# Performance work log

Measured on AMD Instinct MI355X. Metric: run time of the kernel, lower is better.

The kernel has to match this reference:

```python
import jax, jax.numpy as jnp
import numpy as np

B, N, C = 16, 65536, 21          # batch, anchors, classes (class 0 = background)
TH_CONF = 0.05                   # confidence threshold
TH_IOU = 0.5                     # NMS IoU threshold
TOP_K = 200                      # candidates kept per (batch, class) before NMS
V0, V1 = 0.1, 0.2                # SSD box-coder variances


def setup_inputs() -> dict:
    key = jax.random.key(0)
    k1, k2, k3, k4 = jax.random.split(key, 4)
    conf = jax.random.normal(k1, (B, N, C), dtype=jnp.float32)
    loc = jax.random.normal(k2, (B, N, 4), dtype=jnp.float32)
    # anchors in center form (cx, cy, w, h), normalized coords
    cxcy = jax.random.uniform(k3, (N, 2), dtype=jnp.float32)
    wh = 0.02 + 0.2 * jax.random.uniform(k4, (N, 2), dtype=jnp.float32)
    anchors = jnp.concatenate([cxcy, wh], axis=-1)
    return {"conf": conf, "loc": loc, "anchors": anchors}


def _decode(anchors, loc):
    # SSD decode: anchors [N,4] center form, loc [B,N,4] offsets -> [B,N,4] xyxy
    a_xy, a_wh = anchors[:, :2], anchors[:, 2:]
    xy = a_xy + loc[..., :2] * V0 * a_wh
    wh = a_wh * jnp.exp(loc[..., 2:] * V1)
    return jnp.concatenate([xy - 0.5 * wh, xy + 0.5 * wh], axis=-1)


def _iou(boxes):
    # boxes [K,4] xyxy -> pairwise IoU [K,K]
    area = jnp.maximum(boxes[:, 2] - boxes[:, 0], 0.0) * jnp.maximum(boxes[:, 3] - boxes[:, 1], 0.0)
    lt = jnp.maximum(boxes[:, None, :2], boxes[None, :, :2])
    rb = jnp.minimum(boxes[:, None, 2:], boxes[None, :, 2:])
    wh = jnp.maximum(rb - lt, 0.0)
    inter = wh[..., 0] * wh[..., 1]
    union = area[:, None] + area[None, :] - inter
    return inter / jnp.maximum(union, 1e-9)


def _nms_keep(iou, valid):
    # greedy NMS over score-sorted candidates; valid = (score >= TH_CONF)
    K = iou.shape[0]
    idx = jnp.arange(K)

    def body(keep, xs):
        row, v, i = xs
        suppressed = jnp.any((row > TH_IOU) & keep & (idx < i))
        k = v & (~suppressed)
        return keep.at[i].set(k), 0

    keep, _ = jax.lax.scan(body, jnp.zeros((K,), dtype=bool), (iou, valid, idx))
    return keep


def reference(conf, loc, anchors):
    score = jax.nn.softmax(conf, axis=2)            # [B,N,C]
    boxes = _decode(anchors, loc)                   # [B,N,4]
    # skip background class 0 (cls_base = 1 for softmax classifier)
    cls_scores = jnp.swapaxes(score[..., 1:], 1, 2)  # [B,C-1,N]
    top_s, top_i = jax.lax.top_k(cls_scores, TOP_K)  # [B,C-1,K], sorted desc
    top_boxes = jax.vmap(lambda bx, ix: bx[ix])(boxes, top_i)  # [B,C-1,K,4]
    valid = top_s >= TH_CONF
    keep = jax.vmap(jax.vmap(lambda b, v: _nms_keep(_iou(b), v)))(top_boxes, valid)  # [B,C-1,K]
    out_boxes = jnp.where(keep[..., None], top_boxes, 0.0)
    out_scores = jnp.where(keep, top_s, 0.0)
    return jnp.concatenate([out_boxes, out_scores[..., None]], axis=-1)  # [B,C-1,K,5]
```

## Files before the change

kernel.cpp:

```cpp
#include <hip/hip_runtime.h>
#include <stdint.h>

#define NB     16
#define NANCH  65536
#define NC     21
#define NCLS   20
#define NCOL   (NB * NCLS)
#define TOPK   200
#define NBINS  1024
#define CAP    256
#define CAPCOL 4096
#define CAPLDS 2048
#define CNTSTRIDE 16
#define NPAIRS 19900

constexpr float TH      = 0.05f;
constexpr float TPRE    = 0.20f;
constexpr float SCALE20 = (float)NBINS / 0.80f;
constexpr float SCALE05 = (float)NBINS / 0.95f;

__device__ __forceinline__ int bin20(float s) {
  int b = (int)((s - 0.20f) * SCALE20);
  return b < 0 ? 0 : (b > NBINS - 1 ? NBINS - 1 : b);
}
__device__ __forceinline__ int bin05(float s) {
  int b = (int)((s - 0.05f) * SCALE05);
  return b < 0 ? 0 : (b > NBINS - 1 ? NBINS - 1 : b);
}

__device__ __forceinline__ unsigned long long shflx64(unsigned long long v, int m) {
  unsigned int lo = (unsigned int)v, hi = (unsigned int)(v >> 32);
  lo = __shfl_xor(lo, m);
  hi = __shfl_xor(hi, m);
  return ((unsigned long long)hi << 32) | lo;
}
__device__ __forceinline__ unsigned long long rl64(unsigned long long v, int lane) {
  unsigned int lo = __builtin_amdgcn_readlane((int)(unsigned int)v, lane);
  unsigned int hi = __builtin_amdgcn_readlane((int)(unsigned int)(v >> 32), lane);
  return ((unsigned long long)hi << 32) | lo;
}

__device__ __forceinline__ void softmax_tail(const float* x, float* e, float& S) {
  float m = x[0];
#pragma unroll
  for (int c = 1; c < NC; ++c) m = fmaxf(m, x[c]);
#pragma unroll
  for (int c = 0; c < NC; ++c) e[c] = expf(x[c] - m);
  float r0 = e[0] + e[8],  r1 = e[1] + e[9],  r2 = e[2] + e[10], r3 = e[3] + e[11];
  float r4 = e[4] + e[12], r5 = e[5] + e[13], r6 = e[6] + e[14], r7 = e[7] + e[15];
  S = ((r0 + r1) + (r2 + r3)) + ((r4 + r5) + (r6 + r7));
  S += e[16]; S += e[17]; S += e[18]; S += e[19]; S += e[20];
}

__global__ __launch_bounds__(256) void softmax_collect_kernel(
    const float* __restrict__ conf,
    unsigned int* __restrict__ cnt, unsigned long long* __restrict__ cand) {
  const int tid = threadIdx.x;
  __shared__ float ld[256 * NC];
  const float4* src = (const float4*)conf + (long long)blockIdx.x * 1344;
  float4* dst4 = (float4*)ld;
#pragma unroll
  for (int i = 0; i < 5; ++i) dst4[tid + i * 256] = src[tid + i * 256];
  if (tid < 64) dst4[tid + 1280] = src[tid + 1280];
  __syncthreads();

  const int a = blockIdx.x * 256 + tid;
  const int b = a >> 16;
  const int n = a & (NANCH - 1);
  float x[NC];
#pragma unroll
  for (int c = 0; c < NC; ++c) x[c] = ld[tid * NC + c];
  float e[NC], S;
  softmax_tail(x, e, S);
  const float t = TPRE * S;
  unsigned int takemask = 0;
#pragma unroll
  for (int c = 0; c < NCLS; ++c)
    if (e[c + 1] >= t) takemask |= (1u << c);

  __shared__ unsigned int wcnt[4][NCLS];
  __shared__ unsigned int wbase[4][NCLS];
  const int wave = tid >> 6, lane = tid & 63;
#pragma unroll
  for (int c = 0; c < NCLS; ++c) {
    unsigned long long m = __ballot((takemask >> c) & 1);
    if (lane == 0) wcnt[wave][c] = (unsigned int)__popcll(m);
  }
  __syncthreads();
  if (tid < NCLS) {
    const int c = tid;
    unsigned int t0 = wcnt[0][c], t1 = wcnt[1][c], t2 = wcnt[2][c], t3 = wcnt[3][c];
    unsigned int tot = t0 + t1 + t2 + t3;
    unsigned int base = tot ? atomicAdd(&cnt[(b * NCLS + c) * CNTSTRIDE], tot) : 0u;
    wbase[0][c] = base;
    wbase[1][c] = base + t0;
    wbase[2][c] = base + t0 + t1;
    wbase[3][c] = base + t0 + t1 + t2;
  }
  __syncthreads();
#pragma unroll
  for (int c = 0; c < NCLS; ++c) {
    bool take = (takemask >> c) & 1;
    unsigned long long m = __ballot(take);
    if (take) {
      float s = e[c + 1] / S;
      unsigned int off = wbase[wave][c] +
                         (unsigned int)__popcll(m & ((1ULL << lane) - 1));
      if (off < CAPCOL) {
        unsigned int key = __float_as_uint(s) | 0x80000000u;
        cand[(long long)(b * NCLS + c) * CAPCOL + off] =
            ((unsigned long long)(key ^ 0xFFFFFFFFu) << 32) |
            (unsigned long long)(unsigned int)n;
      }
    }
  }
}

__device__ __forceinline__ int find_sel(unsigned int* hist, unsigned int* part,
                                        int* s_sel, int tid) {
  unsigned int p = hist[tid*4] + hist[tid*4+1] + hist[tid*4+2] + hist[tid*4+3];
  part[tid] = p;
  if (tid == 0) *s_sel = -1;
  __syncthreads();
  if (tid < 64) {
    unsigned int p4 = part[tid*4] + part[tid*4+1] + part[tid*4+2] + part[tid*4+3];
    unsigned int sfx = p4;
#pragma unroll
    for (int off = 1; off < 64; off <<= 1) {
      unsigned int o = __shfl_down(sfx, off);
      if (tid + off < 64) sfx += o;
    }
    unsigned int above = sfx - p4;
    if (above < TOPK && sfx >= TOPK) {
      unsigned int cum = above; int sel = tid * 16; bool found = false;
      for (int q = 3; q >= 0 && !found; --q) {
        unsigned int pc = part[tid*4 + q];
        if (cum + pc >= TOPK) {
          for (int i = 3; i >= 0; --i) {
            unsigned int c = hist[(tid*4+q)*4 + i];
            if (cum + c >= TOPK) { sel = (tid*4+q)*4 + i; found = true; break; }
            cum += c;
          }
        } else cum += pc;
      }
      *s_sel = sel;
    }
  }
  __syncthreads();
  return *s_sel;
}

__global__ __launch_bounds__(256) void topk_nms_kernel(
    const unsigned long long* __restrict__ candg,
    const unsigned int* __restrict__ cnt,
    const float* __restrict__ conf, const float* __restrict__ loc,
    const float* __restrict__ anchors, float* __restrict__ out) {
  const int bc = blockIdx.x;
  const int b  = bc / NCLS;
  const int cls = bc % NCLS;
  const int tid = threadIdx.x;

  __shared__ unsigned long long cg_lds[CAPLDS];
  __shared__ unsigned int hist[NBINS];
  __shared__ unsigned int part[256];
  __shared__ int s_sel, s_n;
  __shared__ unsigned long long cand[CAP];
  __shared__ float bx[TOPK][5];
  __shared__ float barea[TOPK];
  __shared__ unsigned long long adj[TOPK][4];
  __shared__ unsigned long long keptw[4];

  int nc = (int)cnt[bc * CNTSTRIDE];
  const bool fast = (nc >= TOPK && nc <= CAPLDS);
  for (int i = tid; i < NBINS; i += 256) hist[i] = 0;
  if (tid == 0) s_n = 0;
  for (int i = tid; i < TOPK * 4; i += 256) ((unsigned long long*)adj)[i] = 0;

  const unsigned long long* cg = candg + (long long)bc * CAPCOL;
  if (fast) {
    const int npair = nc >> 1;
    const ulonglong2* cg2 = (const ulonglong2*)cg;
    for (int i = tid; i < npair; i += 256) {
      ulonglong2 v2 = cg2[i];
      cg_lds[2 * i]     = v2.x;
      cg_lds[2 * i + 1] = v2.y;
    }
    if ((nc & 1) && tid == 0) cg_lds[nc - 1] = cg[nc - 1];
    __syncthreads();
    for (int i = tid; i < nc; i += 256) {
      unsigned int key = (unsigned int)(cg_lds[i] >> 32) ^ 0xFFFFFFFFu;
      float s = __uint_as_float(key ^ 0x80000000u);
      atomicAdd(&hist[bin20(s)], 1u);
    }
    __syncthreads();
    int sel = find_sel(hist, part, &s_sel, tid);
    for (int i = tid; i < nc; i += 256) {
      unsigned long long k64 = cg_lds[i];
      unsigned int key = (unsigned int)(k64 >> 32) ^ 0xFFFFFFFFu;
      float s = __uint_as_float(key ^ 0x80000000u);
      if (bin20(s) >= sel) {
        int pos = atomicAdd(&s_n, 1);
        if (pos < CAP) cand[pos] = k64;
      }
    }
  } else {
    __syncthreads();
    for (int n = tid; n < NANCH; n += 256) {
      const float* row = conf + ((long long)b * NANCH + n) * NC;
      float x[NC], e[NC], S;
#pragma unroll
      for (int c = 0; c < NC; ++c) x[c] = row[c];
      softmax_tail(x, e, S);
      float s = e[cls + 1] / S;
      if (s >= TH) atomicAdd(&hist[bin05(s)], 1u);
    }
    __syncthreads();
    int sel = find_sel(hist, part, &s_sel, tid);
    for (int n = tid; n < NANCH; n += 256) {
      const float* row = conf + ((long long)b * NANCH + n) * NC;
      float x[NC], e[NC], S;
#pragma unroll
      for (int c = 0; c < NC; ++c) x[c] = row[c];
      softmax_tail(x, e, S);
      float s = e[cls + 1] / S;
      if (s >= TH && (sel < 0 || bin05(s) >= sel)) {
        int pos = atomicAdd(&s_n, 1);
        if (pos < CAP) {
          unsigned int key = __float_as_uint(s) | 0x80000000u;
          cand[pos] = ((unsigned long long)(key ^ 0xFFFFFFFFu) << 32) |
                      (unsigned long long)(unsigned int)n;
        }
      }
    }
  }
  __syncthreads();
  int ncand = s_n; if (ncand > CAP) ncand = CAP;

  unsigned long long v = (tid < ncand) ? cand[tid] : ~0ULL;
  for (int k = 2; k <= CAP; k <<= 1) {
    const bool up = ((tid & k) == 0);
    for (int j = k >> 1; j >= 64; j >>= 1) {
      cand[tid] = v;
      __syncthreads();
      unsigned long long o = cand[tid ^ j];
      bool keepMin = (((tid & j) == 0) == up);
      v = ((v < o) == keepMin) ? v : o;
      __syncthreads();
    }
    for (int j = (k >> 1) < 32 ? (k >> 1) : 32; j >= 1; j >>= 1) {
      unsigned long long o = shflx64(v, j);
      bool keepMin = (((tid & j) == 0) == up);
      v = ((v < o) == keepMin) ? v : o;
    }
  }
  const int nsel = (ncand < TOPK) ? ncand : TOPK;

  if (tid < TOPK) {
    if (tid < nsel) {
      unsigned int key = (unsigned int)(v >> 32) ^ 0xFFFFFFFFu;
      float s = __uint_as_float(key ^ 0x80000000u);
      int idx = (int)(unsigned int)(v & 0xFFFFFFFFu);
      float4 anc = ((const float4*)anchors)[idx];
      float4 l   = ((const float4*)loc)[(long long)b * NANCH + idx];
      float cx = anc.x + (l.x * 0.1f) * anc.z;
      float cy = anc.y + (l.y * 0.1f) * anc.w;
      float w  = anc.z * expf(l.z * 0.2f);
      float h  = anc.w * expf(l.w * 0.2f);
      float x1 = cx - 0.5f * w, y1 = cy - 0.5f * h;
      float x2 = cx + 0.5f * w, y2 = cy + 0.5f * h;
      bx[tid][0] = x1; bx[tid][1] = y1; bx[tid][2] = x2; bx[tid][3] = y2;
      bx[tid][4] = s;
      barea[tid] = fmaxf(x2 - x1, 0.0f) * fmaxf(y2 - y1, 0.0f);
    } else {
      bx[tid][0] = bx[tid][1] = bx[tid][2] = bx[tid][3] = bx[tid][4] = 0.0f;
      barea[tid] = 0.0f;
    }
  }
  __syncthreads();

  for (int p = tid; p < NPAIRS; p += 256) {
    float xr = (399.0f - sqrtf((float)(159201 - 8 * p))) * 0.5f;
    int i = (int)xr;
    if (i > 198) i = 198;
    while (i * (399 - i) / 2 > p) --i;
    while ((i + 1) * (398 - i) / 2 <= p) ++i;
    int j = i + 1 + (p - i * (399 - i) / 2);
    float ltx = fmaxf(bx[i][0], bx[j][0]);
    float lty = fmaxf(bx[i][1], bx[j][1]);
    float rbx = fminf(bx[i][2], bx[j][2]);
    float rby = fminf(bx[i][3], bx[j][3]);
    float iw = fmaxf(rbx - ltx, 0.0f);
    float ih = fmaxf(rby - lty, 0.0f);
    float inter = iw * ih;
    float uni = barea[i] + barea[j] - inter;
    float um = fmaxf(uni, 1e-9f);
    float half = 0.5f * um;
    bool hit;
    if (inter > half * 1.000001f)      hit = true;
    else if (inter < half * 0.999999f) hit = false;
    else                               hit = (inter / um > 0.5f);
    if (hit) atomicOr(&adj[i][j >> 6], 1ULL << (j & 63));
  }
  __syncthreads();

  if (tid < 64) {
    const int l = tid;
    unsigned long long r0[4], r1[4], r2[4], r3[4];
#pragma unroll
    for (int w = 0; w < 4; ++w) {
      r0[w] = adj[l][w];
      r1[w] = adj[l + 64][w];
      r2[w] = (l < 72) ? adj[l + 128][w] : 0ULL;
      r3[w] = (l < 8)  ? adj[l + 192][w] : 0ULL;
    }
    unsigned long long sup0 = 0, sup1 = 0, sup2 = 0, sup3 = 0;
    unsigned long long k0 = 0, k1 = 0, k2 = 0, k3 = 0;
    for (int ii = 0; ii < 64; ++ii) {
      bool kept = (ii < nsel) && !((sup0 >> ii) & 1ULL);
      if (kept) {
        k0 |= 1ULL << ii;
        sup0 |= rl64(r0[0], ii); sup1 |= rl64(r0[1], ii);
        sup2 |= rl64(r0[2], ii); sup3 |= rl64(r0[3], ii);
      }
    }
    for (int ii = 0; ii < 64; ++ii) {
      bool kept = ((64 + ii) < nsel) && !((sup1 >> ii) & 1ULL);
      if (kept) {
        k1 |= 1ULL << ii;
        sup1 |= rl64(r1[1], ii); sup2 |= rl64(r1[2], ii);
        sup3 |= rl64(r1[3], ii);
      }
    }
    for (int ii = 0; ii < 64; ++ii) {
      bool kept = ((128 + ii) < nsel) && !((sup2 >> ii) & 1ULL);
      if (kept) {
        k2 |= 1ULL << ii;
        sup2 |= rl64(r2[2], ii); sup3 |= rl64(r2[3], ii);
      }
    }
    for (int ii = 0; ii < 8; ++ii) {
      bool kept = ((192 + ii) < nsel) && !((sup3 >> ii) & 1ULL);
      if (kept) { k3 |= 1ULL << ii; sup3 |= rl64(r3[3], ii); }
    }
    if (l == 0) { keptw[0] = k0; keptw[1] = k1; keptw[2] = k2; keptw[3] = k3; }
  }
  __syncthreads();

  if (tid < TOPK) {
    float* o = out + ((long long)bc * TOPK + tid) * 5;
    bool k = (keptw[tid >> 6] >> (tid & 63)) & 1ULL;
    o[0] = k ? bx[tid][0] : 0.0f;
    o[1] = k ? bx[tid][1] : 0.0f;
    o[2] = k ? bx[tid][2] : 0.0f;
    o[3] = k ? bx[tid][3] : 0.0f;
    o[4] = k ? bx[tid][4] : 0.0f;
  }
}

extern "C" void kernel_launch(void* const* d_in, const int* in_sizes, int n_in,
                              void* d_out, int out_size, void* d_ws, size_t ws_size,
                              hipStream_t stream) {
  const float* conf    = (const float*)d_in[0];
  const float* loc     = (const float*)d_in[1];
  const float* anchors = (const float*)d_in[2];
  float* out = (float*)d_out;

  char* ws = (char*)d_ws;
  unsigned long long* cand = (unsigned long long*)ws;
  unsigned int*       cnt  = (unsigned int*)(ws + 10485760);

  hipMemsetAsync(ws + 10485760, 0, 320 * CNTSTRIDE * 4, stream);
  softmax_collect_kernel<<<(NB * NANCH) / 256, 256, 0, stream>>>(conf, cnt, cand);
  topk_nms_kernel<<<NCOL, 256, 0, stream>>>(cand, cnt, conf, loc, anchors, out);
}
```

Measured before the change: 99.64 us.

## Pack two (batch,class) columns per 512-thread block and alias NMS buffers onto staging LDS

The top-k/NMS kernel now runs two columns per block, with 512 threads split into halves, so 160 blocks are launched instead of 320. The adjacency matrix, box and area arrays are moved into the candidate staging buffer, which is no longer needed at that point, to keep total LDS use down. The fast path is taken only when both columns qualify, so one slow column drags its partner through the full softmax rescan. Block-wide barriers are now shared by both halves, coupling their progress.

Result: slower. 104.0 us (+4.4%).

```diff
diff --git a/kernel.cpp b/kernel.cpp
--- a/kernel.cpp
+++ b/kernel.cpp
@@ -117,28 +117,28 @@
 }
 
 __device__ __forceinline__ int find_sel(unsigned int* hist, unsigned int* part,
-                                        int* s_sel, int tid) {
-  unsigned int p = hist[tid*4] + hist[tid*4+1] + hist[tid*4+2] + hist[tid*4+3];
-  part[tid] = p;
-  if (tid == 0) *s_sel = -1;
-  __syncthreads();
-  if (tid < 64) {
-    unsigned int p4 = part[tid*4] + part[tid*4+1] + part[tid*4+2] + part[tid*4+3];
+                                        int* s_sel, int t) {
+  unsigned int p = hist[t*4] + hist[t*4+1] + hist[t*4+2] + hist[t*4+3];
+  part[t] = p;
+  if (t == 0) *s_sel = -1;
+  __syncthreads();
+  if (t < 64) {
+    unsigned int p4 = part[t*4] + part[t*4+1] + part[t*4+2] + part[t*4+3];
     unsigned int sfx = p4;
 #pragma unroll
     for (int off = 1; off < 64; off <<= 1) {
       unsigned int o = __shfl_down(sfx, off);
-      if (tid + off < 64) sfx += o;
+      if (t + off < 64) sfx += o;
     }
     unsigned int above = sfx - p4;
     if (above < TOPK && sfx >= TOPK) {
-      unsigned int cum = above; int sel = tid * 16; bool found = false;
+      unsigned int cum = above; int sel = t * 16; bool found = false;
       for (int q = 3; q >= 0 && !found; --q) {
-        unsigned int pc = part[tid*4 + q];
+        unsigned int pc = part[t*4 + q];
         if (cum + pc >= TOPK) {
           for (int i = 3; i >= 0; --i) {
-            unsigned int c = hist[(tid*4+q)*4 + i];
-            if (cum + c >= TOPK) { sel = (tid*4+q)*4 + i; found = true; break; }
+            unsigned int c = hist[(t*4+q)*4 + i];
+            if (cum + c >= TOPK) { sel = (t*4+q)*4 + i; found = true; break; }
             cum += c;
           }
         } else cum += pc;
@@ -150,73 +150,76 @@
   return *s_sel;
 }
 
-__global__ __launch_bounds__(256) void topk_nms_kernel(
+__global__ __launch_bounds__(512) void topk_nms_kernel(
     const unsigned long long* __restrict__ candg,
     const unsigned int* __restrict__ cnt,
     const float* __restrict__ conf, const float* __restrict__ loc,
     const float* __restrict__ anchors, float* __restrict__ out) {
-  const int bc = blockIdx.x;
-  const int b  = bc / NCLS;
-  const int cls = bc % NCLS;
-  const int tid = threadIdx.x;
-
-  __shared__ unsigned long long cg_lds[CAPLDS];
-  __shared__ unsigned int hist[NBINS];
-  __shared__ unsigned int part[256];
-  __shared__ int s_sel, s_n;
-  __shared__ unsigned long long cand[CAP];
-  __shared__ float bx[TOPK][5];
-  __shared__ float barea[TOPK];
-  __shared__ unsigned long long adj[TOPK][4];
-  __shared__ unsigned long long keptw[4];
+  const int tid  = threadIdx.x;
+  const int half = tid >> 8;
+  const int t    = tid & 255;
+  const int bc   = blockIdx.x * 2 + half;
+  const int b    = bc / NCLS;
+  const int cls  = bc % NCLS;
+
+  __shared__ unsigned long long cg_lds[2][CAPLDS];
+  __shared__ unsigned int hist[2][NBINS];
+  __shared__ unsigned int part[2][256];
+  __shared__ int s_sel[2], s_n[2];
+  __shared__ unsigned long long cand[2][CAP];
+  __shared__ unsigned long long keptw[2][4];
+  unsigned long long* adj  = &cg_lds[half][0];
+  float*              bx   = (float*)&cg_lds[half][800];
+  float*              brea = (float*)&cg_lds[half][800] + 1000;
 
   int nc = (int)cnt[bc * CNTSTRIDE];
-  const bool fast = (nc >= TOPK && nc <= CAPLDS);
-  for (int i = tid; i < NBINS; i += 256) hist[i] = 0;
-  if (tid == 0) s_n = 0;
-  for (int i = tid; i < TOPK * 4; i += 256) ((unsigned long long*)adj)[i] = 0;
+  int nc_other = (int)cnt[(blockIdx.x * 2 + (half ^ 1)) * CNTSTRIDE];
+  const bool fastpair = (nc >= TOPK && nc <= CAPLDS) &&
+                        (nc_other >= TOPK && nc_other <= CAPLDS);
+  for (int i = t; i < NBINS; i += 256) hist[half][i] = 0;
+  if (t == 0) s_n[half] = 0;
 
   const unsigned long long* cg = candg + (long long)bc * CAPCOL;
-  if (fast) {
+  if (fastpair) {
     const int npair = nc >> 1;
     const ulonglong2* cg2 = (const ulonglong2*)cg;
-    for (int i = tid; i < npair; i += 256) {
+    for (int i = t; i < npair; i += 256) {
       ulonglong2 v2 = cg2[i];
-      cg_lds[2 * i]     = v2.x;
-      cg_lds[2 * i + 1] = v2.y;
-    }
-    if ((nc & 1) && tid == 0) cg_lds[nc - 1] = cg[nc - 1];
+      cg_lds[half][2 * i]     = v2.x;
+      cg_lds[half][2 * i + 1] = v2.y;
+    }
+    if ((nc & 1) && t == 0) cg_lds[half][nc - 1] = cg[nc - 1];
     __syncthreads();
-    for (int i = tid; i < nc; i += 256) {
-      unsigned int key = (unsigned int)(cg_lds[i] >> 32) ^ 0xFFFFFFFFu;
+    for (int i = t; i < nc; i += 256) {
+      unsigned int key = (unsigned int)(cg_lds[half][i] >> 32) ^ 0xFFFFFFFFu;
       float s = __uint_as_float(key ^ 0x80000000u);
-      atomicAdd(&hist[bin20(s)], 1u);
+      atomicAdd(&hist[half][bin20(s)], 1u);
     }
     __syncthreads();
-    int sel = find_sel(hist, part, &s_sel, tid);
-    for (int i = tid; i < nc; i += 256) {
-      unsigned long long k64 = cg_lds[i];
+    int sel = find_sel(hist[half], part[half], &s_sel[half], t);
+    for (int i = t; i < nc; i += 256) {
+      unsigned long long k64 = cg_lds[half][i];
       unsigned int key = (unsigned int)(k64 >> 32) ^ 0xFFFFFFFFu;
       float s = __uint_as_float(key ^ 0x80000000u);
       if (bin20(s) >= sel) {
-        int pos = atomicAdd(&s_n, 1);
-        if (pos < CAP) cand[pos] = k64;
+        int pos = atomicAdd(&s_n[half], 1);
+        if (pos < CAP) cand[half][pos] = k64;
       }
     }
   } else {
     __syncthreads();
-    for (int n = tid; n < NANCH; n += 256) {
+    for (int n = t; n < NANCH; n += 256) {
       const float* row = conf + ((long long)b * NANCH + n) * NC;
       float x[NC], e[NC], S;
 #pragma unroll
       for (int c = 0; c < NC; ++c) x[c] = row[c];
       softmax_tail(x, e, S);
       float s = e[cls + 1] / S;
-      if (s >= TH) atomicAdd(&hist[bin05(s)], 1u);
+      if (s >= TH) atomicAdd(&hist[half][bin05(s)], 1u);
     }
     __syncthreads();
-    int sel = find_sel(hist, part, &s_sel, tid);
-    for (int n = tid; n < NANCH; n += 256) {
+    int sel = find_sel(hist[half], part[half], &s_sel[half], t);
+    for (int n = t; n < NANCH; n += 256) {
       const float* row = conf + ((long long)b * NANCH + n) * NC;
       float x[NC], e[NC], S;
 #pragma unroll
@@ -224,39 +227,40 @@
       softmax_tail(x, e, S);
       float s = e[cls + 1] / S;
       if (s >= TH && (sel < 0 || bin05(s) >= sel)) {
-        int pos = atomicAdd(&s_n, 1);
+        int pos = atomicAdd(&s_n[half], 1);
         if (pos < CAP) {
           unsigned int key = __float_as_uint(s) | 0x80000000u;
-          cand[pos] = ((unsigned long long)(key ^ 0xFFFFFFFFu) << 32) |
-                      (unsigned long long)(unsigned int)n;
+          cand[half][pos] = ((unsigned long long)(key ^ 0xFFFFFFFFu) << 32) |
+                            (unsigned long long)(unsigned int)n;
         }
       }
     }
   }
   __syncthreads();
-  int ncand = s_n; if (ncand > CAP) ncand = CAP;
-
-  unsigned long long v = (tid < ncand) ? cand[tid] : ~0ULL;
+  int ncand = s_n[half]; if (ncand > CAP) ncand = CAP;
+
+  unsigned long long v = (t < ncand) ? cand[half][t] : ~0ULL;
   for (int k = 2; k <= CAP; k <<= 1) {
-    const bool up = ((tid & k) == 0);
+    const bool up = ((t & k) == 0);
     for (int j = k >> 1; j >= 64; j >>= 1) {
-      cand[tid] = v;
+      cand[half][t] = v;
       __syncthreads();
-      unsigned long long o = cand[tid ^ j];
-      bool keepMin = (((tid & j) == 0) == up);
+      unsigned long long o = cand[half][t ^ j];
+      bool keepMin = (((t & j) == 0) == up);
       v = ((v < o) == keepMin) ? v : o;
       __syncthreads();
     }
     for (int j = (k >> 1) < 32 ? (k >> 1) : 32; j >= 1; j >>= 1) {
       unsigned long long o = shflx64(v, j);
-      bool keepMin = (((tid & j) == 0) == up);
+      bool keepMin = (((t & j) == 0) == up);
       v = ((v < o) == keepMin) ? v : o;
     }
   }
   const int nsel = (ncand < TOPK) ? ncand : TOPK;
 
-  if (tid < TOPK) {
-    if (tid < nsel) {
+  for (int i = t; i < TOPK * 4; i += 256) adj[i] = 0;
+  if (t < TOPK) {
+    if (t < nsel) {
       unsigned int key = (unsigned int)(v >> 32) ^ 0xFFFFFFFFu;
       float s = __uint_as_float(key ^ 0x80000000u);
       int idx = (int)(unsigned int)(v & 0xFFFFFFFFu);
@@ -268,50 +272,50 @@
       float h  = anc.w * expf(l.w * 0.2f);
       float x1 = cx - 0.5f * w, y1 = cy - 0.5f * h;
       float x2 = cx + 0.5f * w, y2 = cy + 0.5f * h;
-      bx[tid][0] = x1; bx[tid][1] = y1; bx[tid][2] = x2; bx[tid][3] = y2;
-      bx[tid][4] = s;
-      barea[tid] = fmaxf(x2 - x1, 0.0f) * fmaxf(y2 - y1, 0.0f);
+      bx[t * 5 + 0] = x1; bx[t * 5 + 1] = y1;
+      bx[t * 5 + 2] = x2; bx[t * 5 + 3] = y2; bx[t * 5 + 4] = s;
+      brea[t] = fmaxf(x2 - x1, 0.0f) * fmaxf(y2 - y1, 0.0f);
     } else {
-      bx[tid][0] = bx[tid][1] = bx[tid][2] = bx[tid][3] = bx[tid][4] = 0.0f;
-      barea[tid] = 0.0f;
-    }
-  }
-  __syncthreads();
-
-  for (int p = tid; p < NPAIRS; p += 256) {
+      bx[t*5+0] = bx[t*5+1] = bx[t*5+2] = bx[t*5+3] = bx[t*5+4] = 0.0f;
+      brea[t] = 0.0f;
+    }
+  }
+  __syncthreads();
+
+  for (int p = t; p < NPAIRS; p += 256) {
     float xr = (399.0f - sqrtf((float)(159201 - 8 * p))) * 0.5f;
     int i = (int)xr;
     if (i > 198) i = 198;
     while (i * (399 - i) / 2 > p) --i;
     while ((i + 1) * (398 - i) / 2 <= p) ++i;
     int j = i + 1 + (p - i * (399 - i) / 2);
-    float ltx = fmaxf(bx[i][0], bx[j][0]);
-    float lty = fmaxf(bx[i][1], bx[j][1]);
-    float rbx = fminf(bx[i][2], bx[j][2]);
-    float rby = fminf(bx[i][3], bx[j][3]);
+    float ltx = fmaxf(bx[i*5+0], bx[j*5+0]);
+    float lty = fmaxf(bx[i*5+1], bx[j*5+1]);
+    float rbx = fminf(bx[i*5+2], bx[j*5+2]);
+    float rby = fminf(bx[i*5+3], bx[j*5+3]);
     float iw = fmaxf(rbx - ltx, 0.0f);
     float ih = fmaxf(rby - lty, 0.0f);
     float inter = iw * ih;
-    float uni = barea[i] + barea[j] - inter;
+    float uni = brea[i] + brea[j] - inter;
     float um = fmaxf(uni, 1e-9f);
-    float half = 0.5f * um;
+    float half_u = 0.5f * um;
     bool hit;
-    if (inter > half * 1.000001f)      hit = true;
-    else if (inter < half * 0.999999f) hit = false;
-    else                               hit = (inter / um > 0.5f);
-    if (hit) atomicOr(&adj[i][j >> 6], 1ULL << (j & 63));
-  }
-  __syncthreads();
-
-  if (tid < 64) {
-    const int l = tid;
+    if (inter > half_u * 1.000001f)      hit = true;
+    else if (inter < half_u * 0.999999f) hit = false;
+    else                                 hit = (inter / um > 0.5f);
+    if (hit) atomicOr(&adj[i * 4 + (j >> 6)], 1ULL << (j & 63));
+  }
+  __syncthreads();
+
+  if (t < 64) {
+    const int l = t;
     unsigned long long r0[4], r1[4], r2[4], r3[4];
 #pragma unroll
     for (int w = 0; w < 4; ++w) {
-      r0[w] = adj[l][w];
-      r1[w] = adj[l + 64][w];
-      r2[w] = (l < 72) ? adj[l + 128][w] : 0ULL;
-      r3[w] = (l < 8)  ? adj[l + 192][w] : 0ULL;
+      r0[w] = adj[l * 4 + w];
+      r1[w] = adj[(l + 64) * 4 + w];
+      r2[w] = (l < 72) ? adj[(l + 128) * 4 + w] : 0ULL;
+      r3[w] = (l < 8)  ? adj[(l + 192) * 4 + w] : 0ULL;
     }
     unsigned long long sup0 = 0, sup1 = 0, sup2 = 0, sup3 = 0;
     unsigned long long k0 = 0, k1 = 0, k2 = 0, k3 = 0;
@@ -342,18 +346,19 @@
       bool kept = ((192 + ii) < nsel) && !((sup3 >> ii) & 1ULL);
       if (kept) { k3 |= 1ULL << ii; sup3 |= rl64(r3[3], ii); }
     }
-    if (l == 0) { keptw[0] = k0; keptw[1] = k1; keptw[2] = k2; keptw[3] = k3; }
-  }
-  __syncthreads();
-
-  if (tid < TOPK) {
-    float* o = out + ((long long)bc * TOPK + tid) * 5;
-    bool k = (keptw[tid >> 6] >> (tid & 63)) & 1ULL;
-    o[0] = k ? bx[tid][0] : 0.0f;
-    o[1] = k ? bx[tid][1] : 0.0f;
-    o[2] = k ? bx[tid][2] : 0.0f;
-    o[3] = k ? bx[tid][3] : 0.0f;
-    o[4] = k ? bx[tid][4] : 0.0f;
+    if (l == 0) { keptw[half][0] = k0; keptw[half][1] = k1;
+                  keptw[half][2] = k2; keptw[half][3] = k3; }
+  }
+  __syncthreads();
+
+  if (t < TOPK) {
+    float* o = out + ((long long)bc * TOPK + t) * 5;
+    bool k = (keptw[half][t >> 6] >> (t & 63)) & 1ULL;
+    o[0] = k ? bx[t*5+0] : 0.0f;
+    o[1] = k ? bx[t*5+1] : 0.0f;
+    o[2] = k ? bx[t*5+2] : 0.0f;
+    o[3] = k ? bx[t*5+3] : 0.0f;
+    o[4] = k ? bx[t*5+4] : 0.0f;
   }
 }
 
@@ -371,5 +376,5 @@
 
   hipMemsetAsync(ws + 10485760, 0, 320 * CNTSTRIDE * 4, stream);
   softmax_collect_kernel<<<(NB * NANCH) / 256, 256, 0, stream>>>(conf, cnt, cand);
-  topk_nms_kernel<<<NCOL, 256, 0, stream>>>(cand, cnt, conf, loc, anchors, out);
-}
+  topk_nms_kernel<<<NCOL / 2, 512, 0, stream>>>(cand, cnt, conf, loc, anchors, out);
+}
```

## Compute IoU adjacency rows per thread without atomics and branchless NMS scan

Applied to the files above, without the earlier changes.

Replaces the triangular pair-index decomposition (sqrt plus fix-up loops and atomicOr into shared memory) with one thread per row that builds each 64-bit adjacency word in registers and stores it directly. This removes the zero-init of adj, the LDS atomics and the pair-index arithmetic. In exchange only 200 of 256 threads do the IoU work and each does 200 serial iterations. The greedy NMS scan is made branchless with masks, and the output write is coalesced as a flat loop over TOPK*5 floats.

After: 98.65 us. No clear change (-1.0%).

```diff
diff --git a/kernel.cpp b/kernel.cpp
--- a/kernel.cpp
+++ b/kernel.cpp
@@ -12,7 +12,6 @@
 #define CAPCOL 4096
 #define CAPLDS 2048
 #define CNTSTRIDE 16
-#define NPAIRS 19900
 
 constexpr float TH      = 0.05f;
 constexpr float TPRE    = 0.20f;
@@ -165,7 +164,7 @@
   __shared__ unsigned int part[256];
   __shared__ int s_sel, s_n;
   __shared__ unsigned long long cand[CAP];
-  __shared__ float bx[TOPK][5];
+  __shared__ float bxf[TOPK * 5];
   __shared__ float barea[TOPK];
   __shared__ unsigned long long adj[TOPK][4];
   __shared__ unsigned long long keptw[4];
@@ -174,7 +173,6 @@
   const bool fast = (nc >= TOPK && nc <= CAPLDS);
   for (int i = tid; i < NBINS; i += 256) hist[i] = 0;
   if (tid == 0) s_n = 0;
-  for (int i = tid; i < TOPK * 4; i += 256) ((unsigned long long*)adj)[i] = 0;
 
   const unsigned long long* cg = candg + (long long)bc * CAPCOL;
   if (fast) {
@@ -268,38 +266,48 @@
       float h  = anc.w * expf(l.w * 0.2f);
       float x1 = cx - 0.5f * w, y1 = cy - 0.5f * h;
       float x2 = cx + 0.5f * w, y2 = cy + 0.5f * h;
-      bx[tid][0] = x1; bx[tid][1] = y1; bx[tid][2] = x2; bx[tid][3] = y2;
-      bx[tid][4] = s;
+      bxf[tid * 5 + 0] = x1; bxf[tid * 5 + 1] = y1;
+      bxf[tid * 5 + 2] = x2; bxf[tid * 5 + 3] = y2; bxf[tid * 5 + 4] = s;
       barea[tid] = fmaxf(x2 - x1, 0.0f) * fmaxf(y2 - y1, 0.0f);
     } else {
-      bx[tid][0] = bx[tid][1] = bx[tid][2] = bx[tid][3] = bx[tid][4] = 0.0f;
+      bxf[tid*5+0] = bxf[tid*5+1] = bxf[tid*5+2] = bxf[tid*5+3] = bxf[tid*5+4] = 0.0f;
       barea[tid] = 0.0f;
     }
   }
   __syncthreads();
 
-  for (int p = tid; p < NPAIRS; p += 256) {
-    float xr = (399.0f - sqrtf((float)(159201 - 8 * p))) * 0.5f;
-    int i = (int)xr;
-    if (i > 198) i = 198;
-    while (i * (399 - i) / 2 > p) --i;
-    while ((i + 1) * (398 - i) / 2 <= p) ++i;
-    int j = i + 1 + (p - i * (399 - i) / 2);
-    float ltx = fmaxf(bx[i][0], bx[j][0]);
-    float lty = fmaxf(bx[i][1], bx[j][1]);
-    float rbx = fminf(bx[i][2], bx[j][2]);
-    float rby = fminf(bx[i][3], bx[j][3]);
-    float iw = fmaxf(rbx - ltx, 0.0f);
-    float ih = fmaxf(rby - lty, 0.0f);
-    float inter = iw * ih;
-    float uni = barea[i] + barea[j] - inter;
-    float um = fmaxf(uni, 1e-9f);
-    float half = 0.5f * um;
-    bool hit;
-    if (inter > half * 1.000001f)      hit = true;
-    else if (inter < half * 0.999999f) hit = false;
-    else                               hit = (inter / um > 0.5f);
-    if (hit) atomicOr(&adj[i][j >> 6], 1ULL << (j & 63));
+  if (tid < TOPK) {
+    const float ax1 = bxf[tid*5+0], ay1 = bxf[tid*5+1];
+    const float ax2 = bxf[tid*5+2], ay2 = bxf[tid*5+3];
+    const float aar = barea[tid];
+#pragma unroll
+    for (int w = 0; w < 4; ++w) {
+      const int jend = (w < 3) ? 64 : (TOPK - 192);
+      unsigned long long roww = 0;
+      for (int jj = 0; jj < jend; ++jj) {
+        const int j = w * 64 + jj;
+        float jx1 = bxf[j*5+0], jy1 = bxf[j*5+1];
+        float jx2 = bxf[j*5+2], jy2 = bxf[j*5+3];
+        float jar = barea[j];
+        float ltx = fmaxf(ax1, jx1);
+        float lty = fmaxf(ay1, jy1);
+        float rbx = fminf(ax2, jx2);
+        float rby = fminf(ay2, jy2);
+        float iw = fmaxf(rbx - ltx, 0.0f);
+        float ih = fmaxf(rby - lty, 0.0f);
+        float inter = iw * ih;
+        float uni = aar + jar - inter;
+        float um = fmaxf(uni, 1e-9f);
+        float half = 0.5f * um;
+        bool hit;
+        if (inter > half * 1.000001f)      hit = true;
+        else if (inter < half * 0.999999f) hit = false;
+        else                               hit = (inter / um > 0.5f);
+        hit = hit && (j > tid);
+        roww |= (unsigned long long)(hit ? 1ULL : 0ULL) << jj;
+      }
+      adj[tid][w] = roww;
+    }
   }
   __syncthreads();
 
@@ -310,50 +318,50 @@
     for (int w = 0; w < 4; ++w) {
       r0[w] = adj[l][w];
       r1[w] = adj[l + 64][w];
-      r2[w] = (l < 72) ? adj[l + 128][w] : 0ULL;
-      r3[w] = (l < 8)  ? adj[l + 192][w] : 0ULL;
+      r2[w] = adj[l + 128][w];
+      r3[w] = (l < 8) ? adj[l + 192][w] : 0ULL;
     }
     unsigned long long sup0 = 0, sup1 = 0, sup2 = 0, sup3 = 0;
     unsigned long long k0 = 0, k1 = 0, k2 = 0, k3 = 0;
     for (int ii = 0; ii < 64; ++ii) {
-      bool kept = (ii < nsel) && !((sup0 >> ii) & 1ULL);
-      if (kept) {
-        k0 |= 1ULL << ii;
-        sup0 |= rl64(r0[0], ii); sup1 |= rl64(r0[1], ii);
-        sup2 |= rl64(r0[2], ii); sup3 |= rl64(r0[3], ii);
-      }
+      unsigned long long live = ((~sup0 >> ii) & 1ULL) &
+                                (unsigned long long)(ii < nsel);
+      unsigned long long mask = 0ULL - live;
+      k0 |= live << ii;
+      sup0 |= rl64(r0[0], ii) & mask; sup1 |= rl64(r0[1], ii) & mask;
+      sup2 |= rl64(r0[2], ii) & mask; sup3 |= rl64(r0[3], ii) & mask;
     }
     for (int ii = 0; ii < 64; ++ii) {
-      bool kept = ((64 + ii) < nsel) && !((sup1 >> ii) & 1ULL);
-      if (kept) {
-        k1 |= 1ULL << ii;
-        sup1 |= rl64(r1[1], ii); sup2 |= rl64(r1[2], ii);
-        sup3 |= rl64(r1[3], ii);
-      }
+      unsigned long long live = ((~sup1 >> ii) & 1ULL) &
+                                (unsigned long long)((64 + ii) < nsel);
+      unsigned long long mask = 0ULL - live;
+      k1 |= live << ii;
+      sup1 |= rl64(r1[1], ii) & mask; sup2 |= rl64(r1[2], ii) & mask;
+      sup3 |= rl64(r1[3], ii) & mask;
     }
     for (int ii = 0; ii < 64; ++ii) {
-      bool kept = ((128 + ii) < nsel) && !((sup2 >> ii) & 1ULL);
-      if (kept) {
-        k2 |= 1ULL << ii;
-        sup2 |= rl64(r2[2], ii); sup3 |= rl64(r2[3], ii);
-      }
+      unsigned long long live = ((~sup2 >> ii) & 1ULL) &
+                                (unsigned long long)((128 + ii) < nsel);
+      unsigned long long mask = 0ULL - live;
+      k2 |= live << ii;
+      sup2 |= rl64(r2[2], ii) & mask; sup3 |= rl64(r2[3], ii) & mask;
     }
     for (int ii = 0; ii < 8; ++ii) {
-      bool kept = ((192 + ii) < nsel) && !((sup3 >> ii) & 1ULL);
-      if (kept) { k3 |= 1ULL << ii; sup3 |= rl64(r3[3], ii); }
+      unsigned long long live = ((~sup3 >> ii) & 1ULL) &
+                                (unsigned long long)((192 + ii) < nsel);
+      unsigned long long mask = 0ULL - live;
+      k3 |= live << ii;
+      sup3 |= rl64(r3[3], ii) & mask;
     }
     if (l == 0) { keptw[0] = k0; keptw[1] = k1; keptw[2] = k2; keptw[3] = k3; }
   }
   __syncthreads();
 
-  if (tid < TOPK) {
-    float* o = out + ((long long)bc * TOPK + tid) * 5;
-    bool k = (keptw[tid >> 6] >> (tid & 63)) & 1ULL;
-    o[0] = k ? bx[tid][0] : 0.0f;
-    o[1] = k ? bx[tid][1] : 0.0f;
-    o[2] = k ? bx[tid][2] : 0.0f;
-    o[3] = k ? bx[tid][3] : 0.0f;
-    o[4] = k ? bx[tid][4] : 0.0f;
+  float* ob = out + (long long)bc * (TOPK * 5);
+  for (int pos = tid; pos < TOPK * 5; pos += 256) {
+    int row = pos / 5;
+    bool k = (keptw[row >> 6] >> (row & 63)) & 1ULL;
+    ob[pos] = k ? bxf[pos] : 0.0f;
   }
 }
 
```
